# Kernel optimization log

Measured on AMD Instinct MI355X. Metric: run time of the kernel, lower is better.

Reference implementation:

```python
import jax, jax.numpy as jnp
import numpy as np

IGNORE_INDEX = -100  # torch default; targets here are all valid but mask is honored
REDUCTION = "mean"

B, D, V = 4096, 2048, 32000


def setup_inputs() -> dict:
    key = jax.random.key(0)
    k1, k2, k3 = jax.random.split(key, 3)
    x = jax.random.normal(k1, (B, D), dtype=jnp.float32)
    # LM-head weight, scaled like typical init
    L = jax.random.normal(k2, (V, D), dtype=jnp.float32) * (1.0 / np.sqrt(D))
    target = jax.random.randint(k3, (B,), 0, V, dtype=jnp.int64)
    class_weight = jnp.ones((V,), dtype=jnp.float32)  # unnormalized per-class weight
    return {"x": x, "L": L, "target": target, "class_weight": class_weight}


def reference(x, L, target, class_weight):
    """Fused linear + weighted cross-entropy (reduction='mean', ignore_index=-100).

    Equivalent math to MyLinearCrossEntropyFunction: the torch code chunks over
    batches/classes/features with an online softmax solely to avoid materializing
    logits; the unchunked math is a single GEMM + stable log-softmax CE.
    """
    # logits: [B, V]
    logits = jnp.einsum("bd,vd->bv", x, L)
    logZ = jax.nn.logsumexp(logits, axis=1)                      # [B]
    valid = target != IGNORE_INDEX                               # [B] bool
    t_safe = jnp.where(valid, target, 0)
    gathered = jnp.take_along_axis(logits, t_safe[:, None], axis=1)[:, 0]  # [B]
    # effective per-sample weight: class weight of target, zeroed where ignored
    wt = jnp.where(valid, class_weight[t_safe], jnp.zeros((), logits.dtype))  # [B]
    per_sample = wt * (logZ - gathered)
    total = per_sample.sum()
    if REDUCTION == "mean":
        return total / wt.sum()
    return total
```

## Files before the change

kernel.cpp:

```cpp
#include <hip/hip_runtime.h>

#define B_ 4096
#define D_ 2048
#define V_ 32000

#define BM 256
#define BN 256
#define BKB 128
#define NT (D_ / BKB)
#define NCHUNK (V_ / 64)

typedef __attribute__((ext_vector_type(8))) int   int8v;
typedef __attribute__((ext_vector_type(4))) int   int4v;
typedef __attribute__((ext_vector_type(4))) float f32x4;

#define SCALE_A 127
#define SCALE_B 121

__device__ __forceinline__ void load_lds16(const void* g, void* l) {
    __builtin_amdgcn_global_load_lds(
        (const __attribute__((address_space(1))) void*)g,
        (__attribute__((address_space(3))) void*)l,
        16, 0, 0);
}

__device__ __forceinline__ int8v frag(const unsigned char* buf, int base, int p0, int p1) {
    union { int8v v8; int4v v4[2]; } u;
    u.v4[0] = *(const int4v*)(buf + base + p0);
    u.v4[1] = *(const int4v*)(buf + base + p1);
    return u.v8;
}

__global__ void cast_f32_to_fp8(const float* __restrict__ x,
                                const float* __restrict__ L,
                                unsigned int* __restrict__ xq,
                                unsigned int* __restrict__ Lq) {
    const int n4x = (B_ * D_) / 4;
    const int n4l = (V_ * D_) / 4;
    int i = blockIdx.x * blockDim.x + threadIdx.x;
    const float* in; unsigned int* out; float ps; int j;
    if (i < n4x) { in = x; out = xq; ps = 1.0f;  j = i; }
    else         { j = i - n4x; if (j >= n4l) return; in = L; out = Lq; ps = 64.0f; }
    float4 v = ((const float4*)in)[j];
    int w = __builtin_amdgcn_cvt_pk_fp8_f32(v.x * ps, v.y * ps, 0, false);
    w     = __builtin_amdgcn_cvt_pk_fp8_f32(v.z * ps, v.w * ps, w, true);
    out[j] = (unsigned)w;
}

__global__ __launch_bounds__(512, 2)
void gemm_ce_partials(const unsigned char* __restrict__ xq,
                      const unsigned char* __restrict__ Lq,
                      const int* __restrict__ targ,
                      float2* __restrict__ partials,
                      float* __restrict__ gathered) {
    __shared__ __align__(16) unsigned char As[2][BM * BKB];
    __shared__ __align__(16) unsigned char Bs[2][BN * BKB];

    const int tid    = threadIdx.x;
    const int lane   = tid & 63;
    const int wid    = tid >> 6;
    const int wave_m = wid >> 2;
    const int wave_n = wid & 3;
    const int quad   = lane >> 4;
    const int l16    = lane & 15;
    const int swz    = l16 & 7;

    const int m0 = blockIdx.x * BM;
    const int n0 = blockIdx.y * BN;

    const int r0 = tid >> 3;
    const int c0 = (tid & 7) ^ (r0 & 7);
    const unsigned char* sA = xq + (size_t)(m0 + r0) * D_ + c0 * 16;
    const unsigned char* sB = Lq + (size_t)(n0 + r0) * D_ + c0 * 16;
    const int d0 = tid * 16;
#define STEP (64 * D_)
#define DSTEP 8192

    f32x4 acc[8][4];
#pragma unroll
    for (int i = 0; i < 8; ++i)
#pragma unroll
        for (int j = 0; j < 4; ++j)
            acc[i][j] = (f32x4){0.f, 0.f, 0.f, 0.f};

    const int p0 = ((quad ^ swz) << 4);
    const int p1 = p0 ^ 64;

    const int arow = (wave_m * 128 + l16) * BKB;
    const int brow = (wave_n * 64 + l16) * BKB;
#define AB(mi) (arow + (mi) * (16 * BKB))
#define BB(ni) (brow + (ni) * (16 * BKB))
#define MM(A, B, MI, NI)                                                     \
    acc[MI][NI] = __builtin_amdgcn_mfma_scale_f32_16x16x128_f8f6f4(          \
        A, B, acc[MI][NI], 0, 0, 0, SCALE_A, 0, SCALE_B)

#pragma unroll
    for (int p = 0; p < 4; ++p) {
        load_lds16(sA + (size_t)p * STEP, &As[0][d0 + p * DSTEP]);
        load_lds16(sB + (size_t)p * STEP, &Bs[0][d0 + p * DSTEP]);
    }
    asm volatile("s_waitcnt vmcnt(0)" ::: "memory");
    __builtin_amdgcn_s_barrier();

    for (int kt = 0; kt < NT; ++kt) {
        const int cur = kt & 1;
        const int nxt = cur ^ 1;
        const size_t k1 = (size_t)(kt + 1) * BKB;
        const bool pf = (kt + 1 < NT);
        const unsigned char* Ac = As[cur];
        const unsigned char* Bc = Bs[cur];

        int8v a0, a1, a2, a3, b0, b1, b2, b3, s;

        a0 = frag(Ac, AB(0), p0, p1);
        a1 = frag(Ac, AB(1), p0, p1);
        b0 = frag(Bc, BB(0), p0, p1);
        a2 = frag(Ac, AB(2), p0, p1);
        a3 = frag(Ac, AB(3), p0, p1);
        b1 = frag(Bc, BB(1), p0, p1);
        if (pf) {
            load_lds16(sB + k1, &Bs[nxt][d0]);
            load_lds16(sB + k1 + (size_t)STEP, &Bs[nxt][d0 + DSTEP]);
        }
        __builtin_amdgcn_s_barrier();
        __builtin_amdgcn_s_setprio(1);
        MM(a0, b0, 0, 0); MM(a1, b0, 1, 0);
        __builtin_amdgcn_s_setprio(0);

        b2 = frag(Bc, BB(2), p0, p1);
        b3 = frag(Bc, BB(3), p0, p1);
        s  = frag(Ac, AB(4), p0, p1);
        if (pf) {
            load_lds16(sB + k1 + (size_t)2 * STEP, &Bs[nxt][d0 + 2 * DSTEP]);
            load_lds16(sB + k1 + (size_t)3 * STEP, &Bs[nxt][d0 + 3 * DSTEP]);
        }
        __builtin_amdgcn_s_barrier();
        __builtin_amdgcn_s_setprio(1);
        MM(a2, b0, 2, 0); MM(a3, b0, 3, 0);
        MM(a0, b1, 0, 1); MM(a1, b1, 1, 1); MM(a2, b1, 2, 1); MM(a3, b1, 3, 1);
        __builtin_amdgcn_s_setprio(0);

        if (pf) {
            load_lds16(sA + k1, &As[nxt][d0]);
            load_lds16(sA + k1 + (size_t)STEP, &As[nxt][d0 + DSTEP]);
        }
        __builtin_amdgcn_s_barrier();
        __builtin_amdgcn_s_setprio(1);
        MM(a0, b2, 0, 2); MM(a1, b2, 1, 2); MM(a2, b2, 2, 2); MM(a3, b2, 3, 2);
        MM(a0, b3, 0, 3); MM(a1, b3, 1, 3); MM(a2, b3, 2, 3); MM(a3, b3, 3, 3);
        __builtin_amdgcn_s_setprio(0);

        a0 = frag(Ac, AB(5), p0, p1);
        a1 = frag(Ac, AB(6), p0, p1);
        a2 = frag(Ac, AB(7), p0, p1);
        if (pf) {
            load_lds16(sA + k1 + (size_t)2 * STEP, &As[nxt][d0 + 2 * DSTEP]);
            load_lds16(sA + k1 + (size_t)3 * STEP, &As[nxt][d0 + 3 * DSTEP]);
        }
        __builtin_amdgcn_s_barrier();
        __builtin_amdgcn_s_setprio(1);
        MM(s, b0, 4, 0); MM(s, b1, 4, 1); MM(s, b2, 4, 2); MM(s, b3, 4, 3);
        MM(a0, b0, 5, 0); MM(a0, b1, 5, 1); MM(a0, b2, 5, 2); MM(a0, b3, 5, 3);
        MM(a1, b0, 6, 0); MM(a1, b1, 6, 1); MM(a1, b2, 6, 2); MM(a1, b3, 6, 3);
        MM(a2, b0, 7, 0); MM(a2, b1, 7, 1); MM(a2, b2, 7, 2); MM(a2, b3, 7, 3);
        __builtin_amdgcn_s_setprio(0);
        asm volatile("s_waitcnt vmcnt(0)" ::: "memory");
        __builtin_amdgcn_s_barrier();
    }

    const int row_base = m0 + wave_m * 128;
    const int col_base = n0 + wave_n * 64;
    const int chunk    = blockIdx.y * 4 + wave_n;

    int tv[32];
#pragma unroll
    for (int mi = 0; mi < 8; ++mi)
#pragma unroll
        for (int r = 0; r < 4; ++r)
            tv[mi * 4 + r] = targ[row_base + mi * 16 + quad * 4 + r];

    float M = acc[0][0][0];
#pragma unroll
    for (int mi = 0; mi < 8; ++mi)
#pragma unroll
        for (int ni = 0; ni < 4; ++ni)
#pragma unroll
            for (int r = 0; r < 4; ++r)
                M = fmaxf(M, acc[mi][ni][r]);
#pragma unroll
    for (int off = 1; off < 64; off <<= 1)
        M = fmaxf(M, __shfl_xor(M, off, 64));

    float sv[32];
#pragma unroll
    for (int mi = 0; mi < 8; ++mi)
#pragma unroll
        for (int r = 0; r < 4; ++r)
            sv[mi * 4 + r] = __expf(acc[mi][0][r] - M) + __expf(acc[mi][1][r] - M) +
                             __expf(acc[mi][2][r] - M) + __expf(acc[mi][3][r] - M);
#pragma unroll
    for (int off = 1; off < 16; off <<= 1)
#pragma unroll
        for (int i = 0; i < 32; ++i)
            sv[i] += __shfl_xor(sv[i], off, 64);

    if (l16 == 0) {
#pragma unroll
        for (int mi = 0; mi < 8; ++mi)
#pragma unroll
            for (int r = 0; r < 4; ++r) {
                int row = row_base + mi * 16 + quad * 4 + r;
                partials[(size_t)row * NCHUNK + chunk] = make_float2(M, sv[mi * 4 + r]);
            }
    }

#pragma unroll
    for (int mi = 0; mi < 8; ++mi)
#pragma unroll
        for (int r = 0; r < 4; ++r) {
            int row = row_base + mi * 16 + quad * 4 + r;
            int cb  = col_base + l16;
            int t   = tv[mi * 4 + r];
            if (cb      == t) gathered[row] = acc[mi][0][r];
            if (cb + 16 == t) gathered[row] = acc[mi][1][r];
            if (cb + 32 == t) gathered[row] = acc[mi][2][r];
            if (cb + 48 == t) gathered[row] = acc[mi][3][r];
        }
}

__global__ void combine_rows(const float2* __restrict__ partials,
                             const float* __restrict__ gathered,
                             const int* __restrict__ targ,
                             const float* __restrict__ cw,
                             float* __restrict__ row_loss,
                             float* __restrict__ row_w) {
    int row  = blockIdx.x * 4 + (threadIdx.x >> 6);
    int lane = threadIdx.x & 63;
    float m = -3.0e38f, s = 0.f;
    for (int c = lane; c < NCHUNK; c += 64) {
        float2 p = partials[(size_t)row * NCHUNK + c];
        float nm = fmaxf(m, p.x);
        s = s * __expf(m - nm) + p.y * __expf(p.x - nm);
        m = nm;
    }
#pragma unroll
    for (int off = 32; off; off >>= 1) {
        float om = __shfl_xor(m, off, 64);
        float os = __shfl_xor(s, off, 64);
        float nm = fmaxf(m, om);
        s = s * __expf(m - nm) + os * __expf(om - nm);
        m = nm;
    }
    if (lane == 0) {
        float logZ = m + __logf(s);
        int t = targ[row];
        bool valid = (t != -100);
        int ts = valid ? t : 0;
        float w = valid ? cw[ts] : 0.f;
        row_loss[row] = w * (logZ - gathered[row]);
        row_w[row]    = w;
    }
}

__global__ void final_reduce(const float* __restrict__ rl,
                             const float* __restrict__ rw,
                             float* __restrict__ out) {
    __shared__ float sl[4], sw[4];
    float a = 0.f, b = 0.f;
    for (int i = threadIdx.x; i < B_; i += 256) { a += rl[i]; b += rw[i]; }
#pragma unroll
    for (int off = 32; off; off >>= 1) {
        a += __shfl_xor(a, off, 64);
        b += __shfl_xor(b, off, 64);
    }
    int w = threadIdx.x >> 6;
    if ((threadIdx.x & 63) == 0) { sl[w] = a; sw[w] = b; }
    __syncthreads();
    if (threadIdx.x == 0) {
        float ta = sl[0] + sl[1] + sl[2] + sl[3];
        float tb = sw[0] + sw[1] + sw[2] + sw[3];
        out[0] = ta / tb;
    }
}

extern "C" void kernel_launch(void* const* d_in, const int* in_sizes, int n_in,
                              void* d_out, int out_size, void* d_ws, size_t ws_size,
                              hipStream_t stream) {
    const float* x  = (const float*)d_in[0];
    const float* L  = (const float*)d_in[1];
    const int* targ = (const int*)d_in[2];
    const float* cw = (const float*)d_in[3];
    float* out = (float*)d_out;

    char* ws = (char*)d_ws;
    size_t o = 0;
    unsigned char* xq = (unsigned char*)(ws + o);  o += (size_t)B_ * D_;
    unsigned char* Lq = (unsigned char*)(ws + o);  o += (size_t)V_ * D_;
    float2* partials = (float2*)(ws + o);          o += (size_t)B_ * NCHUNK * 8;
    float* gathered = (float*)(ws + o);            o += (size_t)B_ * 4;
    float* row_loss = (float*)(ws + o);            o += (size_t)B_ * 4;
    float* row_w    = (float*)(ws + o);            o += (size_t)B_ * 4;
    (void)ws_size;

    {
        int n4 = (B_ * D_) / 4 + (V_ * D_) / 4;
        cast_f32_to_fp8<<<(n4 + 255) / 256, 256, 0, stream>>>(
            x, L, (unsigned*)xq, (unsigned*)Lq);
    }

    {
        dim3 grid(B_ / BM, V_ / BN);
        gemm_ce_partials<<<grid, 512, 0, stream>>>(xq, Lq, targ, partials, gathered);
    }

    combine_rows<<<B_ / 4, 256, 0, stream>>>(partials, gathered, targ, cw, row_loss, row_w);

    final_reduce<<<1, 256, 0, stream>>>(row_loss, row_w, out);
}
```

Before: 650.2 us.

## Reschedule MFMA/LDS pipeline, remap GEMM blocks, grid-stride fp8 cast

The GEMM main loop is reordered so next-tile global-to-LDS loads are issued up front and MFMAs proceed in 2x2 sub-blocks with extra barriers between phases. This is meant to overlap fragment loads with matrix math better. Block indices are also remapped with an XCD-aware swizzle so tiles sharing the same L rows run together, to improve L2 reuse. Separately, the fp8 cast kernel becomes a grid-stride loop with a fixed grid. The extra barriers and holding eight A fragments at once add sync and register pressure.

```diff
diff --git a/kernel.cpp b/kernel.cpp
--- a/kernel.cpp
+++ b/kernel.cpp
@@ -37,14 +37,17 @@
                                 unsigned int* __restrict__ Lq) {
     const int n4x = (B_ * D_) / 4;
     const int n4l = (V_ * D_) / 4;
-    int i = blockIdx.x * blockDim.x + threadIdx.x;
-    const float* in; unsigned int* out; float ps; int j;
-    if (i < n4x) { in = x; out = xq; ps = 1.0f;  j = i; }
-    else         { j = i - n4x; if (j >= n4l) return; in = L; out = Lq; ps = 64.0f; }
-    float4 v = ((const float4*)in)[j];
-    int w = __builtin_amdgcn_cvt_pk_fp8_f32(v.x * ps, v.y * ps, 0, false);
-    w     = __builtin_amdgcn_cvt_pk_fp8_f32(v.z * ps, v.w * ps, w, true);
-    out[j] = (unsigned)w;
+    const int total = n4x + n4l;
+    const int stride = gridDim.x * blockDim.x;
+    for (int i = blockIdx.x * blockDim.x + threadIdx.x; i < total; i += stride) {
+        const float* in; unsigned int* out; float ps; int j;
+        if (i < n4x) { in = x; out = xq; ps = 1.0f;  j = i; }
+        else         { in = L; out = Lq; ps = 64.0f; j = i - n4x; }
+        float4 v = ((const float4*)in)[j];
+        int w = __builtin_amdgcn_cvt_pk_fp8_f32(v.x * ps, v.y * ps, 0, false);
+        w     = __builtin_amdgcn_cvt_pk_fp8_f32(v.z * ps, v.w * ps, w, true);
+        out[j] = (unsigned)w;
+    }
 }
 
 __global__ __launch_bounds__(512, 2)
@@ -65,8 +68,11 @@
     const int l16    = lane & 15;
     const int swz    = l16 & 7;
 
-    const int m0 = blockIdx.x * BM;
-    const int n0 = blockIdx.y * BN;
+    const int lin  = blockIdx.x + blockIdx.y * (B_ / BM);
+    const int sidx = (lin & 7) * 250 + (lin >> 3);
+    const int m0 = (sidx & 15) * BM;
+    const int nblk = sidx >> 4;
+    const int n0 = nblk * BN;
 
     const int r0 = tid >> 3;
     const int c0 = (tid & 7) ^ (r0 & 7);
@@ -93,6 +99,9 @@
 #define MM(A, B, MI, NI)                                                     \
     acc[MI][NI] = __builtin_amdgcn_mfma_scale_f32_16x16x128_f8f6f4(          \
         A, B, acc[MI][NI], 0, 0, 0, SCALE_A, 0, SCALE_B)
+#define BAR() __builtin_amdgcn_s_barrier()
+#define PRIO1() __builtin_amdgcn_s_setprio(1)
+#define PRIO0() __builtin_amdgcn_s_setprio(0)
 
 #pragma unroll
     for (int p = 0; p < 4; ++p) {
@@ -100,7 +109,7 @@
         load_lds16(sB + (size_t)p * STEP, &Bs[0][d0 + p * DSTEP]);
     }
     asm volatile("s_waitcnt vmcnt(0)" ::: "memory");
-    __builtin_amdgcn_s_barrier();
+    BAR();
 
     for (int kt = 0; kt < NT; ++kt) {
         const int cur = kt & 1;
@@ -110,67 +119,67 @@
         const unsigned char* Ac = As[cur];
         const unsigned char* Bc = Bs[cur];
 
-        int8v a0, a1, a2, a3, b0, b1, b2, b3, s;
-
+        int8v a0, a1, a2, a3, a4, a5, a6, a7, b0, b1, b2, b3;
+
+        if (pf) {
+            load_lds16(sB + k1,                  &Bs[nxt][d0]);
+            load_lds16(sB + k1 + (size_t)STEP,   &Bs[nxt][d0 + DSTEP]);
+            load_lds16(sA + k1,                  &As[nxt][d0]);
+            load_lds16(sA + k1 + (size_t)STEP,   &As[nxt][d0 + DSTEP]);
+        }
+        b0 = frag(Bc, BB(0), p0, p1);
+        b1 = frag(Bc, BB(1), p0, p1);
         a0 = frag(Ac, AB(0), p0, p1);
         a1 = frag(Ac, AB(1), p0, p1);
-        b0 = frag(Bc, BB(0), p0, p1);
-        a2 = frag(Ac, AB(2), p0, p1);
-        a3 = frag(Ac, AB(3), p0, p1);
-        b1 = frag(Bc, BB(1), p0, p1);
-        if (pf) {
-            load_lds16(sB + k1, &Bs[nxt][d0]);
-            load_lds16(sB + k1 + (size_t)STEP, &Bs[nxt][d0 + DSTEP]);
-        }
-        __builtin_amdgcn_s_barrier();
-        __builtin_amdgcn_s_setprio(1);
-        MM(a0, b0, 0, 0); MM(a1, b0, 1, 0);
-        __builtin_amdgcn_s_setprio(0);
-
-        b2 = frag(Bc, BB(2), p0, p1);
-        b3 = frag(Bc, BB(3), p0, p1);
-        s  = frag(Ac, AB(4), p0, p1);
+        BAR();
+        PRIO1();
+        MM(a0, b0, 0, 0); MM(a0, b1, 0, 1); MM(a1, b0, 1, 0); MM(a1, b1, 1, 1);
+        PRIO0();
+        BAR();
+
         if (pf) {
             load_lds16(sB + k1 + (size_t)2 * STEP, &Bs[nxt][d0 + 2 * DSTEP]);
             load_lds16(sB + k1 + (size_t)3 * STEP, &Bs[nxt][d0 + 3 * DSTEP]);
-        }
-        __builtin_amdgcn_s_barrier();
-        __builtin_amdgcn_s_setprio(1);
-        MM(a2, b0, 2, 0); MM(a3, b0, 3, 0);
-        MM(a0, b1, 0, 1); MM(a1, b1, 1, 1); MM(a2, b1, 2, 1); MM(a3, b1, 3, 1);
-        __builtin_amdgcn_s_setprio(0);
-
-        if (pf) {
-            load_lds16(sA + k1, &As[nxt][d0]);
-            load_lds16(sA + k1 + (size_t)STEP, &As[nxt][d0 + DSTEP]);
-        }
-        __builtin_amdgcn_s_barrier();
-        __builtin_amdgcn_s_setprio(1);
-        MM(a0, b2, 0, 2); MM(a1, b2, 1, 2); MM(a2, b2, 2, 2); MM(a3, b2, 3, 2);
-        MM(a0, b3, 0, 3); MM(a1, b3, 1, 3); MM(a2, b3, 2, 3); MM(a3, b3, 3, 3);
-        __builtin_amdgcn_s_setprio(0);
-
-        a0 = frag(Ac, AB(5), p0, p1);
-        a1 = frag(Ac, AB(6), p0, p1);
-        a2 = frag(Ac, AB(7), p0, p1);
-        if (pf) {
             load_lds16(sA + k1 + (size_t)2 * STEP, &As[nxt][d0 + 2 * DSTEP]);
             load_lds16(sA + k1 + (size_t)3 * STEP, &As[nxt][d0 + 3 * DSTEP]);
         }
-        __builtin_amdgcn_s_barrier();
-        __builtin_amdgcn_s_setprio(1);
-        MM(s, b0, 4, 0); MM(s, b1, 4, 1); MM(s, b2, 4, 2); MM(s, b3, 4, 3);
-        MM(a0, b0, 5, 0); MM(a0, b1, 5, 1); MM(a0, b2, 5, 2); MM(a0, b3, 5, 3);
-        MM(a1, b0, 6, 0); MM(a1, b1, 6, 1); MM(a1, b2, 6, 2); MM(a1, b3, 6, 3);
-        MM(a2, b0, 7, 0); MM(a2, b1, 7, 1); MM(a2, b2, 7, 2); MM(a2, b3, 7, 3);
-        __builtin_amdgcn_s_setprio(0);
+        b2 = frag(Bc, BB(2), p0, p1);
+        b3 = frag(Bc, BB(3), p0, p1);
+        a2 = frag(Ac, AB(2), p0, p1);
+        a3 = frag(Ac, AB(3), p0, p1);
+        BAR();
+        PRIO1();
+        MM(a2, b0, 2, 0); MM(a2, b1, 2, 1); MM(a3, b0, 3, 0); MM(a3, b1, 3, 1);
+        MM(a0, b2, 0, 2); MM(a0, b3, 0, 3); MM(a1, b2, 1, 2); MM(a1, b3, 1, 3);
+        PRIO0();
+        BAR();
+
+        a4 = frag(Ac, AB(4), p0, p1);
+        a5 = frag(Ac, AB(5), p0, p1);
+        BAR();
+        PRIO1();
+        MM(a2, b2, 2, 2); MM(a2, b3, 2, 3); MM(a3, b2, 3, 2); MM(a3, b3, 3, 3);
+        MM(a4, b0, 4, 0); MM(a4, b1, 4, 1); MM(a5, b0, 5, 0); MM(a5, b1, 5, 1);
+        PRIO0();
+        BAR();
+
+        a6 = frag(Ac, AB(6), p0, p1);
+        a7 = frag(Ac, AB(7), p0, p1);
+        BAR();
+        PRIO1();
+        MM(a4, b2, 4, 2); MM(a4, b3, 4, 3); MM(a5, b2, 5, 2); MM(a5, b3, 5, 3);
+        MM(a6, b0, 6, 0); MM(a6, b1, 6, 1); MM(a6, b2, 6, 2); MM(a6, b3, 6, 3);
+        MM(a7, b0, 7, 0); MM(a7, b1, 7, 1); MM(a7, b2, 7, 2); MM(a7, b3, 7, 3);
+        PRIO0();
+        asm volatile("s_waitcnt lgkmcnt(0)" ::: "memory");
+        __builtin_amdgcn_sched_barrier(0);
         asm volatile("s_waitcnt vmcnt(0)" ::: "memory");
-        __builtin_amdgcn_s_barrier();
+        BAR();
     }
 
     const int row_base = m0 + wave_m * 128;
     const int col_base = n0 + wave_n * 64;
-    const int chunk    = blockIdx.y * 4 + wave_n;
+    const int chunk    = nblk * 4 + wave_n;
 
     int tv[32];
 #pragma unroll
@@ -302,11 +311,7 @@
     float* row_w    = (float*)(ws + o);            o += (size_t)B_ * 4;
     (void)ws_size;
 
-    {
-        int n4 = (B_ * D_) / 4 + (V_ * D_) / 4;
-        cast_f32_to_fp8<<<(n4 + 255) / 256, 256, 0, stream>>>(
-            x, L, (unsigned*)xq, (unsigned*)Lq);
-    }
+    cast_f32_to_fp8<<<4096, 256, 0, stream>>>(x, L, (unsigned*)xq, (unsigned*)Lq);
 
     {
         dim3 grid(B_ / BM, V_ / BN);
```

After: 768.4 us. 18.2% more time.
